# Performance work log

Hardware: AMD Instinct MI355X
Metric: run time of the kernel (lower is better)

## Reference

```python
import jax, jax.numpy as jnp
import numpy as np

B, L, H, W = 4, 16, 4096, 128   # W == nfeat == nclass (required by out.reshape)
NHID = 256

def setup_inputs() -> dict:
    key = jax.random.key(0)
    k1, k2, k3, k4 = jax.random.split(key, 4)
    x = jax.random.normal(k1, (B, L, H, W), dtype=jnp.float32)
    # row-normalized-ish dense adjacency stand-in for the sparse normalized adj
    adj = jax.random.uniform(k2, (H, H), dtype=jnp.float32) / H
    # GraphConvolution params: support = input @ Wk; out = adj @ support + bk
    W1 = jax.random.normal(k3, (W, NHID), dtype=jnp.float32) / np.sqrt(W)
    b1 = jnp.zeros((NHID,), dtype=jnp.float32)
    W2 = jax.random.normal(k4, (NHID, W), dtype=jnp.float32) / np.sqrt(NHID)
    b2 = jnp.zeros((W,), dtype=jnp.float32)
    return {"x": x, "adj": adj, "W1": W1, "b1": b1, "W2": W2, "b2": b2}

def reference(x, adj, W1, b1, W2, b2):
    Bv, Lv, Hv, Wv = x.shape
    xf = x.reshape(Bv * Lv, Hv, Wv)                      # [BL, H, F]
    # gc1: transform then aggregate, fused over all slices (replaces per-slice loop)
    h = jnp.einsum('nm,bmf->bnf', adj, xf @ W1) + b1     # [BL, H, nhid]
    h = jax.nn.relu(h)
    # dropout: inference mode (training=False) -> identity
    out = jnp.einsum('nm,bmf->bnf', adj, h @ W2) + b2    # [BL, H, nclass]
    out = out.reshape(Bv, Lv, Hv, Wv)
    return jax.nn.log_softmax(out, axis=-1)
```

## Files before the change

### kernel.cpp

```cpp
#include <hip/hip_runtime.h>

typedef __attribute__((ext_vector_type(4))) float f32x4;
typedef __attribute__((ext_vector_type(16))) float f32x16;
typedef __attribute__((ext_vector_type(4))) int i32x4;
typedef __attribute__((ext_vector_type(8))) int i32x8;
typedef union { i32x8 v8; i32x4 v4[2]; } opnd;

__device__ __forceinline__ unsigned fp4q(float v) {
  float a = __builtin_fabsf(v);
  unsigned q = (unsigned)(a > 0.25f) + (a > 0.75f) + (a > 1.25f) + (a > 1.75f)
             + (a > 2.5f) + (a > 3.5f) + (a > 5.0f);
  return q | (v < 0.0f ? 8u : 0u);
}

#if __has_builtin(__builtin_amdgcn_cvt_scalef32_pk_fp4_f32)
#define PKFP4(old, x, y, s) __builtin_amdgcn_cvt_scalef32_pk_fp4_f32((old), (x), (y), 1.0f, (s))
#else
#define PKFP4(old, x, y, s) ((old) | ((fp4q(x) | (fp4q(y) << 4)) << (8 * (s))))
#endif

__device__ __forceinline__ long tiled_addr(long r, long k, int nkb) {
  return (((r >> 5) * nkb) + (k >> 6)) * 2048 + ((k & 16) ? 1024 : 0)
       + (((r & 31) + (((k >> 5) & 1) << 5)) << 4) + (k & 15);
}
__device__ __forceinline__ long tile4_addr(long r, long k, int nkb) {
  return (((r >> 5) * nkb) + (k >> 6)) * 1024
       + (((r & 31) + (((k >> 5) & 1) << 5)) << 4) + ((k & 31) >> 1);
}

__device__ __forceinline__ long remap_wg(int lin, int nwg, int gx) {
  long g = lin;
  if ((nwg & 7) == 0) {
    int cpx = nwg >> 3;
    int gyx = cpx / gx;
    int xcd = lin & 7, idx = lin >> 3;
    if ((gx & 3) == 0 && gyx >= 4 && (gyx & 3) == 0) {
      int st = idx >> 4, wi = idx & 15;
      int nstr = gx >> 2;
      int str = st % nstr, stc = st / nstr;
      int r = str * 4 + (wi & 3);
      int c2 = stc * 4 + (wi >> 2);
      g = (long)xcd * cpx + (long)c2 * gx + r;
    } else {
      g = (long)xcd * cpx + idx;
    }
  }
  return g;
}

__global__ __launch_bounds__(256) void cvtAdj4t(const float* __restrict__ in,
                                                unsigned char* __restrict__ out, long n) {
  long i = ((long)blockIdx.x * 256 + threadIdx.x) * 8;
  if (i >= n) return;
  float4 a = *(const float4*)(in + i);
  float4 b = *(const float4*)(in + i + 4);
  const float S = 24576.0f;
  unsigned word = PKFP4(0u, a.x * S, a.y * S, 0);
  word = PKFP4(word, a.z * S, a.w * S, 1);
  word = PKFP4(word, b.x * S, b.y * S, 2);
  word = PKFP4(word, b.z * S, b.w * S, 3);
  long r = i >> 12;
  long k = i & 4095;
  *(int*)(out + tile4_addr(r, k, 64)) = (int)word;
}

__global__ __launch_bounds__(256) void cvtX4t(const float* __restrict__ X,
                                              unsigned char* __restrict__ out4) {
  __shared__ float tile[32][33];
  const int tid = threadIdx.x;
  const long bl = blockIdx.z;
  const int m0 = blockIdx.y * 32;
  const int w0 = blockIdx.x * 32;
  const float* xb = X + (bl * 4096 + m0) * 128 + w0;
  int row = tid >> 3, cg = tid & 7;
  float4 v = *(const float4*)(xb + (long)row * 128 + cg * 4);
  tile[row][cg * 4 + 0] = v.x;
  tile[row][cg * 4 + 1] = v.y;
  tile[row][cg * 4 + 2] = v.z;
  tile[row][cg * 4 + 3] = v.w;
  __syncthreads();
  if (tid < 128) {
    int wv = tid & 31, mg = tid >> 5;
    float t[8];
#pragma unroll
    for (int i = 0; i < 8; ++i) t[i] = tile[mg * 8 + i][wv];
    unsigned word = PKFP4(0u, t[0], t[1], 0);
    word = PKFP4(word, t[2], t[3], 1);
    word = PKFP4(word, t[4], t[5], 2);
    word = PKFP4(word, t[6], t[7], 3);
    long r = bl * 128 + w0 + wv;
    long k = m0 + mg * 8;
    *(int*)(out4 + tile4_addr(r, k, 64)) = (int)word;
  }
}

__global__ __launch_bounds__(256) void prep_params(const float* __restrict__ W1,
                                                   const float* __restrict__ W2,
                                                   unsigned char* __restrict__ W1T8,
                                                   unsigned char* __restrict__ W2T8) {
  int idx = blockIdx.x * 256 + threadIdx.x;
  if (idx < 32768) {
    int f = idx >> 7, wv = idx & 127;
    float v = W1[wv * 256 + f] * 16.0f;
    int pk = __builtin_amdgcn_cvt_pk_fp8_f32(v, v, 0, 0);
    W1T8[tiled_addr(f, wv, 2)] = (unsigned char)(pk & 0xff);
  } else {
    int t = idx - 32768;
    int cc = t >> 8, f = t & 255;
    float v = W2[f * 128 + cc] * 16.0f;
    int pk = __builtin_amdgcn_cvt_pk_fp8_f32(v, v, 0, 0);
    W2T8[tiled_addr(cc, f, 4)] = (unsigned char)(pk & 0xff);
  }
}

__global__ __launch_bounds__(256, 3) void gemmS1(const unsigned char* __restrict__ A4,
                                                 const unsigned char* __restrict__ X4,
                                                 const unsigned char* __restrict__ W1T8,
                                                 const unsigned char* __restrict__ W2T8,
                                                 unsigned char* __restrict__ t2T4,
                                                 const float* __restrict__ b1,
                                                 int K, int gx) {
  __shared__ unsigned char S1buf[16384];
  __shared__ unsigned char hbuf[32768];
  __shared__ float b1s[256];
  const int tid = threadIdx.x;
  const int l = tid & 63;
  const int w = tid >> 6;
  b1s[tid] = b1[tid] * 128.0f;
  long g = remap_wg(blockIdx.x, gridDim.x, gx);
  const long row0 = (g % gx) * 128;
  const long bl = g / gx;
  const int nkb = K >> 6;
  const int wr = w >> 1, wc = w & 1;
  const unsigned char* pA = A4 + (((row0 >> 5) + wr * 2) * (long)nkb) * 1024 + l * 16;
  const unsigned char* pB = X4 + ((bl * 4 + wc * 2) * (long)nkb) * 1024 + l * 16;

  f32x16 acc[2][2] = {};
  opnd aA[2], bA[2], aB[2], bB[2];
  const i32x4 z4 = {0, 0, 0, 0};
#pragma unroll
  for (int fi = 0; fi < 2; ++fi) {
    aA[fi].v4[1] = z4; aB[fi].v4[1] = z4;
    bA[fi].v4[1] = z4; bB[fi].v4[1] = z4;
  }

#define LOADG(KT, AV, BV) do { long off_ = (long)(KT) * 1024;                         \
    _Pragma("unroll") for (int fi = 0; fi < 2; ++fi)                                  \
      AV[fi].v4[0] = *(const i32x4*)(pA + (long)fi * nkb * 1024 + off_);              \
    _Pragma("unroll") for (int j = 0; j < 2; ++j)                                     \
      BV[j].v4[0] = *(const i32x4*)(pB + (long)j * nkb * 1024 + off_);                \
  } while (0)

#define MFMAS(AV, BV) do {                                                            \
    __builtin_amdgcn_s_setprio(1);                                                    \
    _Pragma("unroll") for (int fi = 0; fi < 2; ++fi)                                  \
      _Pragma("unroll") for (int j = 0; j < 2; ++j)                                   \
        acc[fi][j] = __builtin_amdgcn_mfma_scale_f32_32x32x64_f8f6f4(                 \
            BV[j].v8, AV[fi].v8, acc[fi][j], 4, 4, 0, 127, 0, 124);                   \
    __builtin_amdgcn_s_setprio(0); } while (0)

  const int nkt = K >> 6;
  LOADG(0, aA, bA);
  int kt = 0;
  for (; kt < nkt - 2; kt += 2) {
    LOADG(kt + 1, aB, bB);
    MFMAS(aA, bA);
    LOADG(kt + 2, aA, bA);
    MFMAS(aB, bB);
  }
  LOADG(nkt - 1, aB, bB);
  MFMAS(aA, bA);
  MFMAS(aB, bB);
#undef LOADG
#undef MFMAS

  const int hi = l >> 5;
  const int ln = l & 31;
#pragma unroll
  for (int fi = 0; fi < 2; ++fi) {
    int n = (wr * 2 + fi) * 32 + ln;
#pragma unroll
    for (int j = 0; j < 2; ++j) {
      int wb = (wc * 2 + j) * 32 + 4 * hi;
#pragma unroll
      for (int r4 = 0; r4 < 4; ++r4) {
        int w0 = wb + 8 * r4;
        int word = __builtin_amdgcn_cvt_pk_fp8_f32(acc[fi][j][4 * r4 + 0],
                                                   acc[fi][j][4 * r4 + 1], 0, false);
        word = __builtin_amdgcn_cvt_pk_fp8_f32(acc[fi][j][4 * r4 + 2],
                                               acc[fi][j][4 * r4 + 3], word, true);
        *(int*)(S1buf + tiled_addr(n, w0, 2)) = word;
      }
    }
  }
  __syncthreads();

  const float c1 = 128.0f / 49152.0f;
#pragma unroll
  for (int hh = 0; hh < 2; ++hh) {
#pragma unroll
    for (int fi = 0; fi < 2; ++fi)
#pragma unroll
      for (int jb = 0; jb < 2; ++jb) acc[fi][jb] = (f32x16){};
#pragma unroll
    for (int kt1 = 0; kt1 < 2; ++kt1) {
#pragma unroll
      for (int jb = 0; jb < 2; ++jb) {
        opnd aw;
        const unsigned char* pW = W1T8 + (long)((hh * 4 + wc * 2 + jb) * 2 + kt1) * 2048 + l * 16;
        aw.v4[0] = *(const i32x4*)(pW);
        aw.v4[1] = *(const i32x4*)(pW + 1024);
#pragma unroll
        for (int fi = 0; fi < 2; ++fi) {
          opnd bs;
          const unsigned char* pS = S1buf + (long)((wr * 2 + fi) * 2 + kt1) * 2048 + l * 16;
          bs.v4[0] = *(const i32x4*)(pS);
          bs.v4[1] = *(const i32x4*)(pS + 1024);
          acc[fi][jb] = __builtin_amdgcn_mfma_scale_f32_32x32x64_f8f6f4(
              aw.v8, bs.v8, acc[fi][jb], 0, 0, 0, 127, 0, 127);
        }
      }
    }
#pragma unroll
    for (int jb = 0; jb < 2; ++jb) {
      int fb = (hh * 4 + wc * 2 + jb) * 32 + 4 * hi;
#pragma unroll
      for (int r4 = 0; r4 < 4; ++r4) {
        int f0 = fb + 8 * r4;
        float4 bb = *(const float4*)(b1s + f0);
#pragma unroll
        for (int fi = 0; fi < 2; ++fi) {
          int n = (wr * 2 + fi) * 32 + ln;
          float v0 = fmaxf(fmaf(acc[fi][jb][4 * r4 + 0], c1, bb.x), 0.0f);
          float v1 = fmaxf(fmaf(acc[fi][jb][4 * r4 + 1], c1, bb.y), 0.0f);
          float v2 = fmaxf(fmaf(acc[fi][jb][4 * r4 + 2], c1, bb.z), 0.0f);
          float v3 = fmaxf(fmaf(acc[fi][jb][4 * r4 + 3], c1, bb.w), 0.0f);
          int word = __builtin_amdgcn_cvt_pk_fp8_f32(v0, v1, 0, false);
          word = __builtin_amdgcn_cvt_pk_fp8_f32(v2, v3, word, true);
          *(int*)(hbuf + tiled_addr(n, f0, 4)) = word;
        }
      }
    }
  }
  __syncthreads();

#pragma unroll
  for (int fi = 0; fi < 2; ++fi)
#pragma unroll
    for (int jb = 0; jb < 2; ++jb) acc[fi][jb] = (f32x16){};
#pragma unroll
  for (int kt2 = 0; kt2 < 4; ++kt2) {
#pragma unroll
    for (int jb = 0; jb < 2; ++jb) {
      opnd bw;
      const unsigned char* pW = W2T8 + (long)((wc * 2 + jb) * 4 + kt2) * 2048 + l * 16;
      bw.v4[0] = *(const i32x4*)(pW);
      bw.v4[1] = *(const i32x4*)(pW + 1024);
#pragma unroll
      for (int fi = 0; fi < 2; ++fi) {
        opnd ah;
        const unsigned char* pH = hbuf + (long)((wr * 2 + fi) * 4 + kt2) * 2048 + l * 16;
        ah.v4[0] = *(const i32x4*)(pH);
        ah.v4[1] = *(const i32x4*)(pH + 1024);
        acc[fi][jb] = __builtin_amdgcn_mfma_scale_f32_32x32x64_f8f6f4(
            ah.v8, bw.v8, acc[fi][jb], 0, 0, 0, 127, 0, 127);
      }
    }
  }
  unsigned char* ob = t2T4 + bl * 262144;
#pragma unroll
  for (int fi = 0; fi < 2; ++fi) {
#pragma unroll
    for (int jb = 0; jb < 2; ++jb) {
      int cc = wc * 64 + jb * 32 + ln;
#pragma unroll
      for (int run = 0; run < 4; ++run) {
        long n0 = row0 + wr * 64 + fi * 32 + 8 * run + 4 * hi;
        const float s = 0.125f;
        unsigned pkw = PKFP4(0u, acc[fi][jb][run * 4 + 0] * s,
                                 acc[fi][jb][run * 4 + 1] * s, 0);
        pkw = PKFP4(pkw, acc[fi][jb][run * 4 + 2] * s,
                         acc[fi][jb][run * 4 + 3] * s, 1);
        *(ushort*)(ob + tile4_addr(cc, n0, 64)) = (ushort)pkw;
      }
    }
  }
}

__global__ __launch_bounds__(512) void gemm256sm(const unsigned char* __restrict__ A4,
                                                 const unsigned char* __restrict__ B4,
                                                 float* __restrict__ out,
                                                 const float* __restrict__ bias,
                                                 float ooScale, int K, int gx,
                                                 int chunkBase) {
  __shared__ unsigned char ring[32768];
  const int tid = threadIdx.x;
  const int l = tid & 63;
  const int w = tid >> 6;
  int lin = blockIdx.x;
  const int nwg = gridDim.x;
  if ((nwg & 7) == 0) {
    int cpx = nwg >> 3;
    lin = (lin & 7) * cpx + (lin >> 3);
  }
  const long row0 = (long)(lin % gx) * 256;
  const long col0 = (long)(lin / gx) * 256;
  const int nkb = K >> 6;
  const unsigned char* sBp = B4 + (((col0 >> 5) + w) * (long)nkb) * 1024 + l * 16;
  unsigned char* ringw = ring + w * 1024;
  const unsigned char* ringr = ring + ((w & 1) * 4) * 1024 + l * 16;
  const unsigned char* pA = A4 + (((row0 + (w >> 1) * 64) >> 5) * (long)nkb) * 1024 + l * 16;

  f32x16 acc[2][4] = {};
  opnd bv[4], a0v[2], a1v[2], a2v[2];
  const i32x4 z4 = {0, 0, 0, 0};
#pragma unroll
  for (int j = 0; j < 4; ++j) bv[j].v4[1] = z4;
#pragma unroll
  for (int fi = 0; fi < 2; ++fi) { a0v[fi].v4[1] = z4; a1v[fi].v4[1] = z4; a2v[fi].v4[1] = z4; }

#define STGB(KT) __builtin_amdgcn_global_load_lds(                                    \
    (const unsigned int*)(const void*)(sBp + (long)(KT) * 1024),                      \
    (unsigned int*)(ringw + (((KT) & 3) << 13)), 16, 0, 0)
#define LOADA(KT, AV) do { long o_ = (long)(KT) * 1024;                               \
    AV[0].v4[0] = *(const i32x4*)(pA + o_);                                           \
    AV[1].v4[0] = *(const i32x4*)(pA + (long)nkb * 1024 + o_); } while (0)
#define LDB(KT) do { const unsigned char* p_ = ringr + (((KT) & 3) << 13);            \
    bv[0].v4[0] = *(const i32x4*)(p_);                                                \
    bv[1].v4[0] = *(const i32x4*)(p_ + 1024);                                         \
    bv[2].v4[0] = *(const i32x4*)(p_ + 2048);                                         \
    bv[3].v4[0] = *(const i32x4*)(p_ + 3072); } while (0)
#define MFMAS(AV) do { __builtin_amdgcn_s_setprio(1);                                 \
    _Pragma("unroll") for (int fi = 0; fi < 2; ++fi)                                  \
      _Pragma("unroll") for (int j = 0; j < 4; ++j)                                   \
        acc[fi][j] = __builtin_amdgcn_mfma_scale_f32_32x32x64_f8f6f4(                 \
            AV[fi].v8, bv[j].v8, acc[fi][j], 4, 4, 0, 127, 0, 127);                   \
    __builtin_amdgcn_s_setprio(0); } while (0)
#define BODY(KT, N, DOSTG, DOA, ALD, AUSE) do {                                       \
    LDB(KT);                                                                          \
    if (DOSTG) STGB((KT) + 3);                                                        \
    if (DOA) LOADA((KT) + 2, ALD);                                                    \
    asm volatile("s_waitcnt vmcnt(" N ")" ::: "memory");                              \
    MFMAS(AUSE);                                                                      \
    __builtin_amdgcn_s_barrier(); } while (0)

  const int nkt = K >> 6;
  STGB(0); STGB(1); STGB(2);
  LOADA(0, a0v); LOADA(1, a1v);
  asm volatile("s_waitcnt vmcnt(6)" ::: "memory");
  __builtin_amdgcn_s_barrier();

  BODY(0, "5", 1, 1, a2v, a0v);
  for (int kt = 1; kt + 6 <= nkt; kt += 3) {
    BODY(kt,     "6", 1, 1, a0v, a1v);
    BODY(kt + 1, "6", 1, 1, a1v, a2v);
    BODY(kt + 2, "6", 1, 1, a2v, a0v);
  }
  BODY(nkt - 3, "5", 0, 1, a0v, a1v);
  BODY(nkt - 2, "2", 0, 0, a0v, a2v);
  BODY(nkt - 1, "0", 0, 0, a0v, a0v);
#undef STGB
#undef LOADA
#undef LDB
#undef MFMAS
#undef BODY

  const int hi = l >> 5;
  const int bl = (int)(col0 >> 7) + (w & 1);
  float bb[4];
#pragma unroll
  for (int j = 0; j < 4; ++j) bb[j] = bias[j * 32 + (l & 31)];
#pragma unroll
  for (int fi = 0; fi < 2; ++fi) {
#pragma unroll
    for (int rr = 0; rr < 16; ++rr) {
      float v0 = acc[fi][0][rr] * ooScale + bb[0];
      float v1 = acc[fi][1][rr] * ooScale + bb[1];
      float v2 = acc[fi][2][rr] * ooScale + bb[2];
      float v3 = acc[fi][3][rr] * ooScale + bb[3];
      float m = fmaxf(fmaxf(v0, v1), fmaxf(v2, v3));
#pragma unroll
      for (int o = 16; o > 0; o >>= 1) m = fmaxf(m, __shfl_xor(m, o));
      float s = __expf(v0 - m) + __expf(v1 - m) + __expf(v2 - m) + __expf(v3 - m);
#pragma unroll
      for (int o = 16; o > 0; o >>= 1) s += __shfl_xor(s, o);
      float lse = m + __logf(s);
      long row = row0 + (w >> 1) * 64 + fi * 32 + ((rr & 3) + 8 * (rr >> 2) + 4 * hi);
      float* dst = out + ((long)(chunkBase + bl) * 4096 + row) * 128;
      dst[(l & 31)] = v0 - lse;
      dst[32 + (l & 31)] = v1 - lse;
      dst[64 + (l & 31)] = v2 - lse;
      dst[96 + (l & 31)] = v3 - lse;
    }
  }
}

extern "C" void kernel_launch(void* const* d_in, const int* in_sizes, int n_in,
                              void* d_out, int out_size, void* d_ws, size_t ws_size,
                              hipStream_t stream) {
  const float* x = (const float*)d_in[0];
  const float* adj = (const float*)d_in[1];
  const float* W1 = (const float*)d_in[2];
  const float* b1 = (const float*)d_in[3];
  const float* W2 = (const float*)d_in[4];
  const float* b2 = (const float*)d_in[5];
  float* out = (float*)d_out;
  char* ws = (char*)d_ws;

  unsigned char* adj4 = (unsigned char*)ws;
  unsigned char* W1T8 = (unsigned char*)(ws + 8388608);
  unsigned char* W2T8 = (unsigned char*)(ws + 8388608 + 32768);
  const size_t base = 9ull * 1024 * 1024;

  const int cands[6] = {64, 32, 16, 8, 4, 2};
  int c = 2;
  for (int t = 0; t < 6; ++t) {
    size_t need = base + (size_t)cands[t] * 524288;
    if (need <= ws_size) { c = cands[t]; break; }
  }
  unsigned char* x4T = (unsigned char*)(ws + base);
  unsigned char* t2T4 = x4T + (size_t)c * 262144;

  cvtAdj4t<<<8192, 256, 0, stream>>>(adj, adj4, (long)4096 * 4096);
  prep_params<<<256, 256, 0, stream>>>(W1, W2, W1T8, W2T8);

  int chunks = 64 / c;
  for (int cb = 0; cb < chunks; ++cb) {
    int base_bl = cb * c;
    const float* xc = x + (long)base_bl * 4096 * 128;

    cvtX4t<<<dim3(4, 128, c), 256, 0, stream>>>(xc, x4T);
    gemmS1<<<32 * c, 256, 0, stream>>>(adj4, x4T, W1T8, W2T8, t2T4, b1, 4096, 32);
    gemm256sm<<<16 * (c / 2), 512, 0, stream>>>(adj4, t2T4, out, b2,
                                                1.0f / 6291456.0f, 4096, 16, base_bl);
  }
}
```

Baseline: 235.0 us.

## Deepen prefetch pipelines and remap workgroups across XCDs in FP4 GEMMs

Deepens the register prefetch in the first GEMM from two to four stages, and in the 256x256 GEMM grows the LDS ring from four to eight stages, prefetching B six tiles ahead and A three tiles ahead. It also adds an XCD-aware workgroup remap for the gx==16 case to improve L2 locality. The goal is to hide more global-memory latency. The cost is more registers and LDS, which may reduce occupancy. The epilogue hardcodes tile indices 55-63, which assumes K=4096 (nkt=64).

```diff
diff --git a/kernel.cpp b/kernel.cpp
--- a/kernel.cpp
+++ b/kernel.cpp
@@ -136,12 +136,12 @@
   const unsigned char* pB = X4 + ((bl * 4 + wc * 2) * (long)nkb) * 1024 + l * 16;
 
   f32x16 acc[2][2] = {};
-  opnd aA[2], bA[2], aB[2], bB[2];
+  opnd aA[2], bA[2], aB[2], bB[2], aC[2], bC[2], aD[2], bD[2];
   const i32x4 z4 = {0, 0, 0, 0};
 #pragma unroll
   for (int fi = 0; fi < 2; ++fi) {
-    aA[fi].v4[1] = z4; aB[fi].v4[1] = z4;
-    bA[fi].v4[1] = z4; bB[fi].v4[1] = z4;
+    aA[fi].v4[1] = z4; aB[fi].v4[1] = z4; aC[fi].v4[1] = z4; aD[fi].v4[1] = z4;
+    bA[fi].v4[1] = z4; bB[fi].v4[1] = z4; bC[fi].v4[1] = z4; bD[fi].v4[1] = z4;
   }
 
 #define LOADG(KT, AV, BV) do { long off_ = (long)(KT) * 1024;                         \
@@ -160,17 +160,16 @@
     __builtin_amdgcn_s_setprio(0); } while (0)
 
   const int nkt = K >> 6;
-  LOADG(0, aA, bA);
+  LOADG(0, aA, bA); LOADG(1, aB, bB); LOADG(2, aC, bC);
   int kt = 0;
-  for (; kt < nkt - 2; kt += 2) {
-    LOADG(kt + 1, aB, bB);
-    MFMAS(aA, bA);
-    LOADG(kt + 2, aA, bA);
-    MFMAS(aB, bB);
-  }
-  LOADG(nkt - 1, aB, bB);
-  MFMAS(aA, bA);
-  MFMAS(aB, bB);
+  for (; kt + 7 < nkt; kt += 4) {
+    LOADG(kt + 3, aD, bD); MFMAS(aA, bA);
+    LOADG(kt + 4, aA, bA); MFMAS(aB, bB);
+    LOADG(kt + 5, aB, bB); MFMAS(aC, bC);
+    LOADG(kt + 6, aC, bC); MFMAS(aD, bD);
+  }
+  LOADG(nkt - 1, aD, bD);
+  MFMAS(aA, bA); MFMAS(aB, bB); MFMAS(aC, bC); MFMAS(aD, bD);
 #undef LOADG
 #undef MFMAS
 
@@ -293,13 +292,19 @@
                                                  const float* __restrict__ bias,
                                                  float ooScale, int K, int gx,
                                                  int chunkBase) {
-  __shared__ unsigned char ring[32768];
+  __shared__ unsigned char ring[65536];
   const int tid = threadIdx.x;
   const int l = tid & 63;
   const int w = tid >> 6;
   int lin = blockIdx.x;
   const int nwg = gridDim.x;
-  if ((nwg & 7) == 0) {
+  if (gx == 16 && (nwg & 63) == 0) {
+    int xcd = lin & 7, idx = lin >> 3;
+    int cpg = nwg >> 6;
+    int r = ((xcd & 1) << 3) + (idx & 7);
+    int c = (xcd >> 1) * cpg + (idx >> 3);
+    lin = c * gx + r;
+  } else if ((nwg & 7) == 0) {
     int cpx = nwg >> 3;
     lin = (lin & 7) * cpx + (lin >> 3);
   }
@@ -312,20 +317,22 @@
   const unsigned char* pA = A4 + (((row0 + (w >> 1) * 64) >> 5) * (long)nkb) * 1024 + l * 16;
 
   f32x16 acc[2][4] = {};
-  opnd bv[4], a0v[2], a1v[2], a2v[2];
+  opnd bv[4], a0v[2], a1v[2], a2v[2], a3v[2];
   const i32x4 z4 = {0, 0, 0, 0};
 #pragma unroll
   for (int j = 0; j < 4; ++j) bv[j].v4[1] = z4;
 #pragma unroll
-  for (int fi = 0; fi < 2; ++fi) { a0v[fi].v4[1] = z4; a1v[fi].v4[1] = z4; a2v[fi].v4[1] = z4; }
+  for (int fi = 0; fi < 2; ++fi) {
+    a0v[fi].v4[1] = z4; a1v[fi].v4[1] = z4; a2v[fi].v4[1] = z4; a3v[fi].v4[1] = z4;
+  }
 
 #define STGB(KT) __builtin_amdgcn_global_load_lds(                                    \
     (const unsigned int*)(const void*)(sBp + (long)(KT) * 1024),                      \
-    (unsigned int*)(ringw + (((KT) & 3) << 13)), 16, 0, 0)
+    (unsigned int*)(ringw + (((KT) & 7) << 13)), 16, 0, 0)
 #define LOADA(KT, AV) do { long o_ = (long)(KT) * 1024;                               \
     AV[0].v4[0] = *(const i32x4*)(pA + o_);                                           \
     AV[1].v4[0] = *(const i32x4*)(pA + (long)nkb * 1024 + o_); } while (0)
-#define LDB(KT) do { const unsigned char* p_ = ringr + (((KT) & 3) << 13);            \
+#define LDB(KT) do { const unsigned char* p_ = ringr + (((KT) & 7) << 13);            \
     bv[0].v4[0] = *(const i32x4*)(p_);                                                \
     bv[1].v4[0] = *(const i32x4*)(p_ + 1024);                                         \
     bv[2].v4[0] = *(const i32x4*)(p_ + 2048);                                         \
@@ -338,27 +345,36 @@
     __builtin_amdgcn_s_setprio(0); } while (0)
 #define BODY(KT, N, DOSTG, DOA, ALD, AUSE) do {                                       \
     LDB(KT);                                                                          \
-    if (DOSTG) STGB((KT) + 3);                                                        \
-    if (DOA) LOADA((KT) + 2, ALD);                                                    \
+    if (DOA) LOADA((KT) + 3, ALD);                                                    \
+    if (DOSTG) STGB((KT) + 6);                                                        \
     asm volatile("s_waitcnt vmcnt(" N ")" ::: "memory");                              \
     MFMAS(AUSE);                                                                      \
     __builtin_amdgcn_s_barrier(); } while (0)
 
   const int nkt = K >> 6;
-  STGB(0); STGB(1); STGB(2);
-  LOADA(0, a0v); LOADA(1, a1v);
-  asm volatile("s_waitcnt vmcnt(6)" ::: "memory");
+  LOADA(0, a0v); LOADA(1, a1v); LOADA(2, a2v);
+  STGB(0); STGB(1); STGB(2); STGB(3); STGB(4); STGB(5);
+  asm volatile("s_waitcnt vmcnt(5)" ::: "memory");
   __builtin_amdgcn_s_barrier();
 
-  BODY(0, "5", 1, 1, a2v, a0v);
-  for (int kt = 1; kt + 6 <= nkt; kt += 3) {
-    BODY(kt,     "6", 1, 1, a0v, a1v);
-    BODY(kt + 1, "6", 1, 1, a1v, a2v);
-    BODY(kt + 2, "6", 1, 1, a2v, a0v);
-  }
-  BODY(nkt - 3, "5", 0, 1, a0v, a1v);
-  BODY(nkt - 2, "2", 0, 0, a0v, a2v);
-  BODY(nkt - 1, "0", 0, 0, a0v, a0v);
+  BODY(0, "7", 1, 1, a3v, a0v);
+  BODY(1, "9", 1, 1, a0v, a1v);
+  BODY(2, "11", 1, 1, a1v, a2v);
+  for (int kt = 3; kt + 9 <= nkt - 1; kt += 4) {
+    BODY(kt,     "10", 1, 1, a2v, a3v);
+    BODY(kt + 1, "10", 1, 1, a3v, a0v);
+    BODY(kt + 2, "10", 1, 1, a0v, a1v);
+    BODY(kt + 3, "10", 1, 1, a1v, a2v);
+  }
+  BODY(55, "10", 1, 1, a2v, a3v);
+  BODY(56, "10", 1, 1, a3v, a0v);
+  BODY(57, "10", 1, 1, a0v, a1v);
+  BODY(58, "9",  0, 1, a1v, a2v);
+  BODY(59, "8",  0, 1, a2v, a3v);
+  BODY(60, "7",  0, 1, a3v, a0v);
+  BODY(61, "4",  0, 0, a0v, a1v);
+  BODY(62, "2",  0, 0, a0v, a2v);
+  BODY(63, "0",  0, 0, a0v, a3v);
 #undef STGB
 #undef LOADA
 #undef LDB
```

Measured after the change: 233.3 us. No clear change (-0.7%).
